# Optimization experiments

Hardware: AMD Instinct MI355X
Metric: run time of the kernel (lower is better)

Reference implementation:

```python
import jax, jax.numpy as jnp
import numpy as np

N = 100000
IN_C = 128
HID = 128
LAT = 64
E = 800000


def gcn_conv(x, src, dst, norm, W, b, num_nodes):
    # x: [N, Cin]; src/dst: [E+N] (self-loops appended); norm: [E+N]
    xw = x @ W                                   # [N, Cout]
    msg = xw[src] * norm[:, None]                # gather + scale, [E+N, Cout]
    out = jax.ops.segment_sum(msg, dst, num_segments=num_nodes)
    return out + b


def setup_inputs() -> dict:
    key = jax.random.key(0)
    ks = jax.random.split(key, 8)
    x = jax.random.normal(ks[0], (N, IN_C), dtype=jnp.float32)
    edge_index = jax.random.randint(ks[1], (2, E), 0, N, dtype=jnp.int64)
    batch = jnp.zeros((N,), dtype=jnp.int64)
    # GCNConv params (Glorot-ish scale)
    W1 = jax.random.normal(ks[2], (IN_C, HID), dtype=jnp.float32) / np.sqrt(IN_C)
    b1 = jnp.zeros((HID,), dtype=jnp.float32)
    Wmu = jax.random.normal(ks[3], (HID, LAT), dtype=jnp.float32) / np.sqrt(HID)
    bmu = jnp.zeros((LAT,), dtype=jnp.float32)
    Wlv = jax.random.normal(ks[4], (HID, LAT), dtype=jnp.float32) / np.sqrt(HID)
    blv = jnp.zeros((LAT,), dtype=jnp.float32)
    return {"x": x, "edge_index": edge_index, "batch": batch,
            "W1": W1, "b1": b1, "Wmu": Wmu, "bmu": bmu, "Wlv": Wlv, "blv": blv}


def reference(x, edge_index, batch, W1, b1, Wmu, bmu, Wlv, blv):
    num_nodes = x.shape[0]
    loop = jnp.arange(num_nodes, dtype=edge_index.dtype)
    src = jnp.concatenate([edge_index[0], loop])   # source nodes (+self loops)
    dst = jnp.concatenate([edge_index[1], loop])   # target nodes (+self loops)
    # symmetric GCN normalization: deg over targets, norm = d[src]^-1/2 * d[dst]^-1/2
    deg = jax.ops.segment_sum(jnp.ones_like(dst, dtype=x.dtype), dst,
                              num_segments=num_nodes)
    dis = jnp.where(deg > 0, jax.lax.rsqrt(deg), 0.0)
    norm = dis[src] * dis[dst]                      # [E+N]

    h = jax.nn.relu(gcn_conv(x, src, dst, norm, W1, b1, num_nodes))
    mu = gcn_conv(h, src, dst, norm, Wmu, bmu, num_nodes)
    logvar = gcn_conv(h, src, dst, norm, Wlv, blv, num_nodes)
    return (mu, logvar)
```

## Files before the change

kernel.cpp:

```cpp
#include <hip/hip_runtime.h>

typedef short bf16x8 __attribute__((ext_vector_type(8)));
typedef float f32x4 __attribute__((ext_vector_type(4)));

#define ELLK 32
#define OCAP 4096
#define CSTRIDE 16

static __device__ __forceinline__ float4 f4zero() { return make_float4(0.f, 0.f, 0.f, 0.f); }

static __device__ __forceinline__ unsigned short f2bf(float f) {
  unsigned u = __float_as_uint(f);
  u += 0x7FFFu + ((u >> 16) & 1u);
  return (unsigned short)(u >> 16);
}
static __device__ __forceinline__ float2 bf2x2(unsigned u) {
  float2 r;
  r.x = __uint_as_float(u << 16);
  r.y = __uint_as_float(u & 0xFFFF0000u);
  return r;
}

__global__ void k_setup(const float* __restrict__ W1, const float* __restrict__ Wmu,
                        const float* __restrict__ Wlv, unsigned short* __restrict__ Wt1,
                        unsigned short* __restrict__ Wt2, uint4* __restrict__ cntz,
                        int* __restrict__ ocount, unsigned* __restrict__ A,
                        unsigned* __restrict__ H, int nz4, int nbz, int n) {
  int b = blockIdx.x;
  if (b < nbz) {
    int i = b * 256 + threadIdx.x;
    if (i < nz4) cntz[i] = make_uint4(0u, 0u, 0u, 0u);
    if (b == 0) {
      int t = threadIdx.x;
      if (t == 0) *ocount = 0;
      if (t < 64) A[(size_t)n * 64 + t] = 0u;
      else if (t < 128) H[(size_t)n * 64 + (t - 64)] = 0u;
    }
  } else {
    int id = (b - nbz) * 256 + threadIdx.x;
    if (id < 16384) {
      int nn = id >> 7, k = id & 127;
      Wt1[id] = f2bf(W1[k * 128 + nn]);
    } else {
      int id2 = id - 16384;
      int nn = id2 >> 7, k = id2 & 127;
      float v = (nn < 64) ? Wmu[k * 64 + nn] : Wlv[k * 64 + (nn - 64)];
      Wt2[id2] = f2bf(v);
    }
  }
}

__global__ void k_fill(const int* __restrict__ ei, int* __restrict__ cnt,
                       int* __restrict__ ell, int2* __restrict__ ovf,
                       int* __restrict__ ocount, int E, int n) {
  int e0 = blockIdx.x * 1024 + threadIdx.x;
  int ss[4], dd[4], pos[4];
  bool ok[4];
#pragma unroll
  for (int k = 0; k < 4; ++k) {
    int e = e0 + k * 256;
    ok[k] = (e < E);
    ss[k] = ok[k] ? ei[e] : 0;
    dd[k] = ok[k] ? ei[E + e] : 0;
  }
#pragma unroll
  for (int k = 0; k < 4; ++k)
    pos[k] = ok[k] ? atomicAdd(&cnt[(size_t)dd[k] * CSTRIDE], 1) : ELLK;
#pragma unroll
  for (int k = 0; k < 4; ++k) {
    if (!ok[k]) continue;
    if (pos[k] < ELLK) {
      __builtin_nontemporal_store(ss[k], &ell[(size_t)pos[k] * n + dd[k]]);
    } else {
      int o = atomicAdd(ocount, 1);
      if (o < OCAP) ovf[o] = make_int2(dd[k], ss[k]);
    }
  }
}

__global__ __launch_bounds__(256) void k_gemm1(
    const float* __restrict__ x, const unsigned short* __restrict__ Wt,
    const int* __restrict__ cnt, unsigned short* __restrict__ A,
    float* __restrict__ dnorm, unsigned* __restrict__ mflag, int n) {
  __shared__ unsigned short Wl[128 * 136];
  __shared__ unsigned short Xl[64 * 136];
  __shared__ float dnl[64];
  const int tid = threadIdx.x;
  const int row0 = blockIdx.x * 64;
  {
    const uint4* Wg = (const uint4*)Wt;
#pragma unroll
    for (int i = 0; i < 8; ++i) {
      int idx = tid + i * 256;
      int r = idx >> 4, c = idx & 15;
      *(uint4*)&Wl[r * 136 + c * 8] = Wg[r * 16 + c];
    }
  }
  {
#pragma unroll
    for (int i = 0; i < 8; ++i) {
      int idx = tid + i * 256;
      int r = idx >> 5, c = idx & 31;
      int gi = row0 + r;
      float4 v = (gi < n) ? ((const float4*)x)[(size_t)gi * 32 + c] : f4zero();
      ushort4 p;
      p.x = f2bf(v.x); p.y = f2bf(v.y); p.z = f2bf(v.z); p.w = f2bf(v.w);
      *(ushort4*)&Xl[r * 136 + c * 4] = p;
    }
  }
  __syncthreads();

  if (tid < 64) {
    int gi = row0 + tid;
    float dn = 0.f;
    if (gi < n) {
      int c = cnt[(size_t)gi * CSTRIDE];
      dn = rsqrtf((float)(c + 1));
      dnorm[gi] = dn;
      int mm = (c < ELLK) ? c : ELLK;
      mflag[gi] = (unsigned)mm | ((c > ELLK) ? 0x80000000u : 0u);
    }
    dnl[tid] = dn;
  }

  const int wave = tid >> 6, lane = tid & 63;
  const int li = lane & 15, quad = lane >> 4;
  const int m0 = wave * 16;
  f32x4 acc[8];
#pragma unroll
  for (int t = 0; t < 8; ++t) acc[t] = (f32x4){0.f, 0.f, 0.f, 0.f};

#pragma unroll
  for (int kk = 0; kk < 4; ++kk) {
    int ko = kk * 32 + quad * 8;
    bf16x8 a = *(const bf16x8*)&Xl[(m0 + li) * 136 + ko];
#pragma unroll
    for (int nt = 0; nt < 8; ++nt) {
      bf16x8 b = *(const bf16x8*)&Wl[(nt * 16 + li) * 136 + ko];
      acc[nt] = __builtin_amdgcn_mfma_f32_16x16x32_bf16(a, b, acc[nt], 0, 0, 0);
    }
  }
  __syncthreads();
  float dn[4];
#pragma unroll
  for (int r = 0; r < 4; ++r) dn[r] = dnl[m0 + quad * 4 + r];
#pragma unroll
  for (int nt = 0; nt < 8; ++nt)
#pragma unroll
    for (int r = 0; r < 4; ++r)
      Xl[(m0 + quad * 4 + r) * 136 + nt * 16 + li] = f2bf(acc[nt][r] * dn[r]);
  __syncthreads();
  {
    uint4* A4 = (uint4*)A;
#pragma unroll
    for (int i = 0; i < 4; ++i) {
      int idx = tid + i * 256;
      int r = idx >> 4, c = idx & 15;
      int gi = row0 + r;
      if (gi < n) A4[(size_t)gi * 16 + c] = *(uint4*)&Xl[r * 136 + c * 8];
    }
  }
}

template <bool EPI_RELU>
__global__ __launch_bounds__(256) void k_spmm(
    const unsigned* __restrict__ mflag, const float* __restrict__ dnorm,
    const int* __restrict__ ell, const int2* __restrict__ ovf,
    const int* __restrict__ ocount, const unsigned* __restrict__ S,
    unsigned* __restrict__ D, const float2* __restrict__ bias, int n) {
  int wid = (blockIdx.x * blockDim.x + threadIdx.x) >> 6;
  if (wid >= n) return;
  int lane = threadIdx.x & 63;

  unsigned mf = mflag[wid];
  int m = (int)(mf & 0xFFFFu);
  float dsd = dnorm[wid];
  float2 acc = bf2x2(S[(size_t)wid * 64 + lane]);

  const int* ep = ell + wid;
  {
    int idx[16];
#pragma unroll
    for (int k = 0; k < 16; ++k) idx[k] = ep[(size_t)k * n];
#pragma unroll
    for (int k = 0; k < 16; ++k) idx[k] = (k < m) ? idx[k] : n;
    unsigned u[16];
#pragma unroll
    for (int k = 0; k < 16; ++k) u[k] = S[(size_t)idx[k] * 64 + lane];
#pragma unroll
    for (int k = 0; k < 16; ++k) {
      float2 f = bf2x2(u[k]);
      acc.x += f.x;
      acc.y += f.y;
    }
  }
  if (m > 16) {
    for (int j0 = 16; j0 < m; j0 += 8) {
      int idx[8];
#pragma unroll
      for (int k = 0; k < 8; ++k) idx[k] = ep[(size_t)(j0 + k) * n];
#pragma unroll
      for (int k = 0; k < 8; ++k) idx[k] = (j0 + k < m) ? idx[k] : n;
      unsigned u[8];
#pragma unroll
      for (int k = 0; k < 8; ++k) u[k] = S[(size_t)idx[k] * 64 + lane];
#pragma unroll
      for (int k = 0; k < 8; ++k) {
        float2 f = bf2x2(u[k]);
        acc.x += f.x;
        acc.y += f.y;
      }
    }
  }
  if (mf & 0x80000000u) {
    int oc = *ocount;
    if (oc > OCAP) oc = OCAP;
    for (int k = 0; k < oc; ++k) {
      int2 e = ovf[k];
      if (e.x == wid) {
        float2 u0 = bf2x2(S[(size_t)e.y * 64 + lane]);
        acc.x += u0.x;
        acc.y += u0.y;
      }
    }
  }
  float2 o;
  if (EPI_RELU) {
    float2 b = bias[lane];
    o.x = dsd * fmaxf(fmaf(dsd, acc.x, b.x), 0.f);
    o.y = dsd * fmaxf(fmaf(dsd, acc.y, b.y), 0.f);
  } else {
    o.x = dsd * acc.x;
    o.y = dsd * acc.y;
  }
  unsigned pk = (unsigned)f2bf(o.x) | ((unsigned)f2bf(o.y) << 16);
  D[(size_t)wid * 64 + lane] = pk;
}

__global__ __launch_bounds__(256) void k_gemm2_mfma(
    const unsigned short* __restrict__ G, const unsigned short* __restrict__ Wt,
    const float* __restrict__ bmu, const float* __restrict__ blv,
    float* __restrict__ out, int n) {
  __shared__ unsigned short Wl[128 * 136];
  __shared__ unsigned short Xl[64 * 136];
  const int tid = threadIdx.x;
  const int row0 = blockIdx.x * 64;
  {
    const uint4* Wg = (const uint4*)Wt;
#pragma unroll
    for (int i = 0; i < 8; ++i) {
      int idx = tid + i * 256;
      int r = idx >> 4, c = idx & 15;
      *(uint4*)&Wl[r * 136 + c * 8] = Wg[r * 16 + c];
    }
  }
  {
    const uint4* Gg = (const uint4*)G;
#pragma unroll
    for (int i = 0; i < 4; ++i) {
      int idx = tid + i * 256;
      int r = idx >> 4, c = idx & 15;
      int gi = row0 + r;
      uint4 v = (gi < n) ? Gg[(size_t)gi * 16 + c] : make_uint4(0, 0, 0, 0);
      *(uint4*)&Xl[r * 136 + c * 8] = v;
    }
  }
  __syncthreads();

  const int wave = tid >> 6, lane = tid & 63;
  const int li = lane & 15, quad = lane >> 4;
  const int m0 = wave * 16;

  float bias[8];
#pragma unroll
  for (int nt = 0; nt < 8; ++nt) {
    int c = nt * 16 + li;
    bias[nt] = (c < 64) ? bmu[c] : blv[c - 64];
  }

  f32x4 acc[8];
#pragma unroll
  for (int t = 0; t < 8; ++t) acc[t] = (f32x4){0.f, 0.f, 0.f, 0.f};

#pragma unroll
  for (int kk = 0; kk < 4; ++kk) {
    int ko = kk * 32 + quad * 8;
    bf16x8 a = *(const bf16x8*)&Xl[(m0 + li) * 136 + ko];
#pragma unroll
    for (int nt = 0; nt < 8; ++nt) {
      bf16x8 b = *(const bf16x8*)&Wl[(nt * 16 + li) * 136 + ko];
      acc[nt] = __builtin_amdgcn_mfma_f32_16x16x32_bf16(a, b, acc[nt], 0, 0, 0);
    }
  }
#pragma unroll
  for (int nt = 0; nt < 8; ++nt) {
    int col = nt * 16 + li;
#pragma unroll
    for (int r = 0; r < 4; ++r) {
      int gi = row0 + m0 + quad * 4 + r;
      if (gi < n) {
        float v = acc[nt][r] + bias[nt];
        if (col < 64) out[(size_t)gi * 64 + col] = v;
        else          out[(size_t)(n + gi) * 64 + (col - 64)] = v;
      }
    }
  }
}

extern "C" void kernel_launch(void* const* d_in, const int* in_sizes, int n_in,
                              void* d_out, int out_size, void* d_ws, size_t ws_size,
                              hipStream_t stream) {
  const float* x   = (const float*)d_in[0];
  const int*   ei  = (const int*)d_in[1];
  const float* W1  = (const float*)d_in[3];
  const float* b1  = (const float*)d_in[4];
  const float* Wmu = (const float*)d_in[5];
  const float* bmu = (const float*)d_in[6];
  const float* Wlv = (const float*)d_in[7];
  const float* blv = (const float*)d_in[8];
  float* out = (float*)d_out;

  const int n = in_sizes[0] / 128;
  const int E = in_sizes[1] / 2;

  float* ws = (float*)d_ws;
  size_t p = 0;
  int* cnt    = (int*)(ws + p); p += (size_t)n * CSTRIDE;
  int* ocount = (int*)(ws + p); p += 1;
  p = (p + 3) & ~(size_t)3;
  int* ell    = (int*)(ws + p); p += (size_t)n * ELLK;
  int2* ovf   = (int2*)(ws + p); p += (size_t)OCAP * 2;
  unsigned* A = (unsigned*)(ws + p); p += (size_t)(n + 1) * 64;
  unsigned* H = (unsigned*)(ws + p); p += (size_t)(n + 1) * 64;
  unsigned* G = (unsigned*)(ws + p); p += (size_t)n * 64;
  unsigned short* Wt1 = (unsigned short*)(ws + p); p += 8192;
  unsigned short* Wt2 = (unsigned short*)(ws + p); p += 8192;
  float* dnorm    = (float*)(ws + p); p += n;
  unsigned* mflag = (unsigned*)(ws + p); p += n;

  int nz4  = (n * CSTRIDE) / 4;
  int nbz  = (nz4 + 255) / 256;
  int eb   = (E + 1023) / 1024;
  int gblk = (n + 63) / 64;
  int sblk = (n + 3) / 4;

  k_setup<<<nbz + 128, 256, 0, stream>>>(W1, Wmu, Wlv, Wt1, Wt2, (uint4*)cnt, ocount,
                                         A, H, nz4, nbz, n);
  k_fill<<<eb, 256, 0, stream>>>(ei, cnt, ell, ovf, ocount, E, n);
  k_gemm1<<<gblk, 256, 0, stream>>>(x, Wt1, cnt, (unsigned short*)A, dnorm, mflag, n);
  k_spmm<true><<<sblk, 256, 0, stream>>>(mflag, dnorm, ell, ovf, ocount, A, H,
                                         (const float2*)b1, n);
  k_spmm<false><<<sblk, 256, 0, stream>>>(mflag, dnorm, ell, ovf, ocount, H, G, nullptr, n);
  k_gemm2_mfma<<<gblk, 256, 0, stream>>>((const unsigned short*)G, Wt2, bmu, blv, out, n);
}
```

Baseline: 294.9 us.

## Fuse edge fill with first GEMM and move source normalization into SpMM

Merges the ELL fill kernel and the first GEMM into one launch, with separate block ranges, so the fill and the dense matmul can run concurrently. Because the GEMM no longer waits for degree counts, the source-side normalization moves into the first SpMM, which gathers dnorm per neighbor, and a small k_dnorm kernel computes norms and flags. Weights are pre-swizzled into MFMA fragment order and read straight from global memory instead of being staged in LDS. The first SpMM loop is simplified to uniform 8-wide batches. The cost is extra dnorm gathers per edge in layer 1 and one added kernel launch.

```diff
diff --git a/kernel.cpp b/kernel.cpp
--- a/kernel.cpp
+++ b/kernel.cpp
@@ -39,63 +39,57 @@
   } else {
     int id = (b - nbz) * 256 + threadIdx.x;
     if (id < 16384) {
-      int nn = id >> 7, k = id & 127;
+      int j = id & 7, lane = (id >> 3) & 63, g = id >> 9;
+      int kk = g >> 3, nt = g & 7, li = lane & 15, quad = lane >> 4;
+      int nn = nt * 16 + li, k = kk * 32 + quad * 8 + j;
       Wt1[id] = f2bf(W1[k * 128 + nn]);
     } else {
       int id2 = id - 16384;
-      int nn = id2 >> 7, k = id2 & 127;
+      int j = id2 & 7, lane = (id2 >> 3) & 63, g = id2 >> 9;
+      int kk = g >> 3, nt = g & 7, li = lane & 15, quad = lane >> 4;
+      int nn = nt * 16 + li, k = kk * 32 + quad * 8 + j;
       float v = (nn < 64) ? Wmu[k * 64 + nn] : Wlv[k * 64 + (nn - 64)];
       Wt2[id2] = f2bf(v);
     }
   }
 }
 
-__global__ void k_fill(const int* __restrict__ ei, int* __restrict__ cnt,
-                       int* __restrict__ ell, int2* __restrict__ ovf,
-                       int* __restrict__ ocount, int E, int n) {
-  int e0 = blockIdx.x * 1024 + threadIdx.x;
-  int ss[4], dd[4], pos[4];
-  bool ok[4];
-#pragma unroll
-  for (int k = 0; k < 4; ++k) {
-    int e = e0 + k * 256;
-    ok[k] = (e < E);
-    ss[k] = ok[k] ? ei[e] : 0;
-    dd[k] = ok[k] ? ei[E + e] : 0;
-  }
-#pragma unroll
-  for (int k = 0; k < 4; ++k)
-    pos[k] = ok[k] ? atomicAdd(&cnt[(size_t)dd[k] * CSTRIDE], 1) : ELLK;
-#pragma unroll
-  for (int k = 0; k < 4; ++k) {
-    if (!ok[k]) continue;
-    if (pos[k] < ELLK) {
-      __builtin_nontemporal_store(ss[k], &ell[(size_t)pos[k] * n + dd[k]]);
-    } else {
-      int o = atomicAdd(ocount, 1);
-      if (o < OCAP) ovf[o] = make_int2(dd[k], ss[k]);
-    }
-  }
-}
-
-__global__ __launch_bounds__(256) void k_gemm1(
+__global__ __launch_bounds__(256, 4) void k_fill_gemm1(
     const float* __restrict__ x, const unsigned short* __restrict__ Wt,
-    const int* __restrict__ cnt, unsigned short* __restrict__ A,
-    float* __restrict__ dnorm, unsigned* __restrict__ mflag, int n) {
-  __shared__ unsigned short Wl[128 * 136];
+    const int* __restrict__ ei, int* __restrict__ cnt, int* __restrict__ ell,
+    int2* __restrict__ ovf, int* __restrict__ ocount,
+    unsigned short* __restrict__ A, int E, int n, int eb) {
   __shared__ unsigned short Xl[64 * 136];
-  __shared__ float dnl[64];
   const int tid = threadIdx.x;
-  const int row0 = blockIdx.x * 64;
-  {
-    const uint4* Wg = (const uint4*)Wt;
-#pragma unroll
-    for (int i = 0; i < 8; ++i) {
-      int idx = tid + i * 256;
-      int r = idx >> 4, c = idx & 15;
-      *(uint4*)&Wl[r * 136 + c * 8] = Wg[r * 16 + c];
-    }
-  }
+
+  if (blockIdx.x < eb) {
+    int e0 = blockIdx.x * 1024 + tid;
+    int ss[4], dd[4], pos[4];
+    bool ok[4];
+#pragma unroll
+    for (int k = 0; k < 4; ++k) {
+      int e = e0 + k * 256;
+      ok[k] = (e < E);
+      ss[k] = ok[k] ? ei[e] : 0;
+      dd[k] = ok[k] ? ei[E + e] : 0;
+    }
+#pragma unroll
+    for (int k = 0; k < 4; ++k)
+      pos[k] = ok[k] ? atomicAdd(&cnt[(size_t)dd[k] * CSTRIDE], 1) : ELLK;
+#pragma unroll
+    for (int k = 0; k < 4; ++k) {
+      if (!ok[k]) continue;
+      if (pos[k] < ELLK) {
+        __builtin_nontemporal_store(ss[k], &ell[(size_t)pos[k] * n + dd[k]]);
+      } else {
+        int o = atomicAdd(ocount, 1);
+        if (o < OCAP) ovf[o] = make_int2(dd[k], ss[k]);
+      }
+    }
+    return;
+  }
+
+  const int row0 = (blockIdx.x - eb) * 64;
   {
 #pragma unroll
     for (int i = 0; i < 8; ++i) {
@@ -110,22 +104,10 @@
   }
   __syncthreads();
 
-  if (tid < 64) {
-    int gi = row0 + tid;
-    float dn = 0.f;
-    if (gi < n) {
-      int c = cnt[(size_t)gi * CSTRIDE];
-      dn = rsqrtf((float)(c + 1));
-      dnorm[gi] = dn;
-      int mm = (c < ELLK) ? c : ELLK;
-      mflag[gi] = (unsigned)mm | ((c > ELLK) ? 0x80000000u : 0u);
-    }
-    dnl[tid] = dn;
-  }
-
   const int wave = tid >> 6, lane = tid & 63;
   const int li = lane & 15, quad = lane >> 4;
   const int m0 = wave * 16;
+  const bf16x8* Wf = (const bf16x8*)Wt;
   f32x4 acc[8];
 #pragma unroll
   for (int t = 0; t < 8; ++t) acc[t] = (f32x4){0.f, 0.f, 0.f, 0.f};
@@ -134,21 +116,19 @@
   for (int kk = 0; kk < 4; ++kk) {
     int ko = kk * 32 + quad * 8;
     bf16x8 a = *(const bf16x8*)&Xl[(m0 + li) * 136 + ko];
-#pragma unroll
-    for (int nt = 0; nt < 8; ++nt) {
-      bf16x8 b = *(const bf16x8*)&Wl[(nt * 16 + li) * 136 + ko];
-      acc[nt] = __builtin_amdgcn_mfma_f32_16x16x32_bf16(a, b, acc[nt], 0, 0, 0);
-    }
+    bf16x8 bf[8];
+#pragma unroll
+    for (int nt = 0; nt < 8; ++nt) bf[nt] = Wf[(kk * 8 + nt) * 64 + lane];
+#pragma unroll
+    for (int nt = 0; nt < 8; ++nt)
+      acc[nt] = __builtin_amdgcn_mfma_f32_16x16x32_bf16(a, bf[nt], acc[nt], 0, 0, 0);
   }
   __syncthreads();
-  float dn[4];
-#pragma unroll
-  for (int r = 0; r < 4; ++r) dn[r] = dnl[m0 + quad * 4 + r];
 #pragma unroll
   for (int nt = 0; nt < 8; ++nt)
 #pragma unroll
     for (int r = 0; r < 4; ++r)
-      Xl[(m0 + quad * 4 + r) * 136 + nt * 16 + li] = f2bf(acc[nt][r] * dn[r]);
+      Xl[(m0 + quad * 4 + r) * 136 + nt * 16 + li] = f2bf(acc[nt][r]);
   __syncthreads();
   {
     uint4* A4 = (uint4*)A;
@@ -162,7 +142,18 @@
   }
 }
 
-template <bool EPI_RELU>
+__global__ void k_dnorm(const int* __restrict__ cnt, float* __restrict__ dnorm,
+                        unsigned* __restrict__ mflag, int n) {
+  int i = blockIdx.x * 256 + threadIdx.x;
+  if (i > n) return;
+  if (i == n) { dnorm[n] = 0.f; mflag[n] = 0u; return; }
+  int c = cnt[(size_t)i * CSTRIDE];
+  dnorm[i] = rsqrtf((float)(c + 1));
+  int m = (c < ELLK) ? c : ELLK;
+  mflag[i] = (unsigned)m | ((c > ELLK) ? 0x80000000u : 0u);
+}
+
+template <bool L1>
 __global__ __launch_bounds__(256) void k_spmm(
     const unsigned* __restrict__ mflag, const float* __restrict__ dnorm,
     const int* __restrict__ ell, const int2* __restrict__ ovf,
@@ -176,40 +167,30 @@
   int m = (int)(mf & 0xFFFFu);
   float dsd = dnorm[wid];
   float2 acc = bf2x2(S[(size_t)wid * 64 + lane]);
+  if (L1) { acc.x *= dsd; acc.y *= dsd; }
 
   const int* ep = ell + wid;
-  {
-    int idx[16];
-#pragma unroll
-    for (int k = 0; k < 16; ++k) idx[k] = ep[(size_t)k * n];
-#pragma unroll
-    for (int k = 0; k < 16; ++k) idx[k] = (k < m) ? idx[k] : n;
-    unsigned u[16];
-#pragma unroll
-    for (int k = 0; k < 16; ++k) u[k] = S[(size_t)idx[k] * 64 + lane];
-#pragma unroll
-    for (int k = 0; k < 16; ++k) {
+  int nbt = (m + 7) >> 3;
+  for (int b = 0; b < nbt; ++b) {
+    int j0 = b * 8;
+    int idx[8];
+#pragma unroll
+    for (int k = 0; k < 8; ++k) idx[k] = ep[(size_t)(j0 + k) * n];
+#pragma unroll
+    for (int k = 0; k < 8; ++k) idx[k] = (j0 + k < m) ? idx[k] : n;
+    unsigned u[8];
+#pragma unroll
+    for (int k = 0; k < 8; ++k) u[k] = S[(size_t)idx[k] * 64 + lane];
+    float w[8];
+    if (L1) {
+#pragma unroll
+      for (int k = 0; k < 8; ++k) w[k] = dnorm[idx[k]];
+    }
+#pragma unroll
+    for (int k = 0; k < 8; ++k) {
       float2 f = bf2x2(u[k]);
-      acc.x += f.x;
-      acc.y += f.y;
-    }
-  }
-  if (m > 16) {
-    for (int j0 = 16; j0 < m; j0 += 8) {
-      int idx[8];
-#pragma unroll
-      for (int k = 0; k < 8; ++k) idx[k] = ep[(size_t)(j0 + k) * n];
-#pragma unroll
-      for (int k = 0; k < 8; ++k) idx[k] = (j0 + k < m) ? idx[k] : n;
-      unsigned u[8];
-#pragma unroll
-      for (int k = 0; k < 8; ++k) u[k] = S[(size_t)idx[k] * 64 + lane];
-#pragma unroll
-      for (int k = 0; k < 8; ++k) {
-        float2 f = bf2x2(u[k]);
-        acc.x += f.x;
-        acc.y += f.y;
-      }
+      if (L1) { acc.x = fmaf(w[k], f.x, acc.x); acc.y = fmaf(w[k], f.y, acc.y); }
+      else    { acc.x += f.x; acc.y += f.y; }
     }
   }
   if (mf & 0x80000000u) {
@@ -219,13 +200,13 @@
       int2 e = ovf[k];
       if (e.x == wid) {
         float2 u0 = bf2x2(S[(size_t)e.y * 64 + lane]);
-        acc.x += u0.x;
-        acc.y += u0.y;
+        float wv = L1 ? dnorm[e.y] : 1.f;
+        acc.x = fmaf(wv, u0.x, acc.x); acc.y = fmaf(wv, u0.y, acc.y);
       }
     }
   }
   float2 o;
-  if (EPI_RELU) {
+  if (L1) {
     float2 b = bias[lane];
     o.x = dsd * fmaxf(fmaf(dsd, acc.x, b.x), 0.f);
     o.y = dsd * fmaxf(fmaf(dsd, acc.y, b.y), 0.f);
@@ -237,23 +218,13 @@
   D[(size_t)wid * 64 + lane] = pk;
 }
 
-__global__ __launch_bounds__(256) void k_gemm2_mfma(
+__global__ __launch_bounds__(256, 4) void k_gemm2_mfma(
     const unsigned short* __restrict__ G, const unsigned short* __restrict__ Wt,
     const float* __restrict__ bmu, const float* __restrict__ blv,
     float* __restrict__ out, int n) {
-  __shared__ unsigned short Wl[128 * 136];
   __shared__ unsigned short Xl[64 * 136];
   const int tid = threadIdx.x;
   const int row0 = blockIdx.x * 64;
-  {
-    const uint4* Wg = (const uint4*)Wt;
-#pragma unroll
-    for (int i = 0; i < 8; ++i) {
-      int idx = tid + i * 256;
-      int r = idx >> 4, c = idx & 15;
-      *(uint4*)&Wl[r * 136 + c * 8] = Wg[r * 16 + c];
-    }
-  }
   {
     const uint4* Gg = (const uint4*)G;
 #pragma unroll
@@ -270,6 +241,7 @@
   const int wave = tid >> 6, lane = tid & 63;
   const int li = lane & 15, quad = lane >> 4;
   const int m0 = wave * 16;
+  const bf16x8* Wf = (const bf16x8*)Wt;
 
   float bias[8];
 #pragma unroll
@@ -286,11 +258,12 @@
   for (int kk = 0; kk < 4; ++kk) {
     int ko = kk * 32 + quad * 8;
     bf16x8 a = *(const bf16x8*)&Xl[(m0 + li) * 136 + ko];
-#pragma unroll
-    for (int nt = 0; nt < 8; ++nt) {
-      bf16x8 b = *(const bf16x8*)&Wl[(nt * 16 + li) * 136 + ko];
-      acc[nt] = __builtin_amdgcn_mfma_f32_16x16x32_bf16(a, b, acc[nt], 0, 0, 0);
-    }
+    bf16x8 bf[8];
+#pragma unroll
+    for (int nt = 0; nt < 8; ++nt) bf[nt] = Wf[(kk * 8 + nt) * 64 + lane];
+#pragma unroll
+    for (int nt = 0; nt < 8; ++nt)
+      acc[nt] = __builtin_amdgcn_mfma_f32_16x16x32_bf16(a, bf[nt], acc[nt], 0, 0, 0);
   }
 #pragma unroll
   for (int nt = 0; nt < 8; ++nt) {
@@ -335,19 +308,21 @@
   unsigned* G = (unsigned*)(ws + p); p += (size_t)n * 64;
   unsigned short* Wt1 = (unsigned short*)(ws + p); p += 8192;
   unsigned short* Wt2 = (unsigned short*)(ws + p); p += 8192;
-  float* dnorm    = (float*)(ws + p); p += n;
-  unsigned* mflag = (unsigned*)(ws + p); p += n;
+  float* dnorm    = (float*)(ws + p); p += n + 1;
+  unsigned* mflag = (unsigned*)(ws + p); p += n + 1;
 
   int nz4  = (n * CSTRIDE) / 4;
   int nbz  = (nz4 + 255) / 256;
   int eb   = (E + 1023) / 1024;
   int gblk = (n + 63) / 64;
+  int nb   = (n + 256) / 256;
   int sblk = (n + 3) / 4;
 
   k_setup<<<nbz + 128, 256, 0, stream>>>(W1, Wmu, Wlv, Wt1, Wt2, (uint4*)cnt, ocount,
                                          A, H, nz4, nbz, n);
-  k_fill<<<eb, 256, 0, stream>>>(ei, cnt, ell, ovf, ocount, E, n);
-  k_gemm1<<<gblk, 256, 0, stream>>>(x, Wt1, cnt, (unsigned short*)A, dnorm, mflag, n);
+  k_fill_gemm1<<<eb + gblk, 256, 0, stream>>>(x, Wt1, ei, cnt, ell, ovf, ocount,
+                                              (unsigned short*)A, E, n, eb);
+  k_dnorm<<<nb, 256, 0, stream>>>(cnt, dnorm, mflag, n);
   k_spmm<true><<<sblk, 256, 0, stream>>>(mflag, dnorm, ell, ovf, ocount, A, H,
                                          (const float2*)b1, n);
   k_spmm<false><<<sblk, 256, 0, stream>>>(mflag, dnorm, ell, ovf, ocount, H, G, nullptr, n);
```

Result: no change. 295.4 us (+0.2%).

## Fuse second SpMM into GEMM2 and pre-swizzle weights into MFMA fragment order

Applied to the files above, without the earlier changes.

The second sparse aggregation is fused into the final GEMM kernel. Each wave aggregates 16 nodes into shared memory and then runs the MFMA projection, which removes the intermediate G buffer write/read and one kernel launch. Weights are pre-permuted in setup into per-lane MFMA fragment order, so both GEMM kernels load B fragments directly from global/L2 instead of staging a 34KB weight tile in LDS. This lowers LDS use to allow more occupancy (launch_bounds 256,4). The cost is that the fused kernel processes nodes serially per wave, giving less memory-level parallelism than one-wave-per-node SpMM. The SpMM loop is also simplified to uniform 8-wide batches.

```diff
diff --git a/kernel.cpp b/kernel.cpp
--- a/kernel.cpp
+++ b/kernel.cpp
@@ -39,11 +39,15 @@
   } else {
     int id = (b - nbz) * 256 + threadIdx.x;
     if (id < 16384) {
-      int nn = id >> 7, k = id & 127;
+      int j = id & 7, lane = (id >> 3) & 63, g = id >> 9;
+      int kk = g >> 3, nt = g & 7, li = lane & 15, quad = lane >> 4;
+      int nn = nt * 16 + li, k = kk * 32 + quad * 8 + j;
       Wt1[id] = f2bf(W1[k * 128 + nn]);
     } else {
       int id2 = id - 16384;
-      int nn = id2 >> 7, k = id2 & 127;
+      int j = id2 & 7, lane = (id2 >> 3) & 63, g = id2 >> 9;
+      int kk = g >> 3, nt = g & 7, li = lane & 15, quad = lane >> 4;
+      int nn = nt * 16 + li, k = kk * 32 + quad * 8 + j;
       float v = (nn < 64) ? Wmu[k * 64 + nn] : Wlv[k * 64 + (nn - 64)];
       Wt2[id2] = f2bf(v);
     }
@@ -78,24 +82,14 @@
   }
 }
 
-__global__ __launch_bounds__(256) void k_gemm1(
+__global__ __launch_bounds__(256, 4) void k_gemm1(
     const float* __restrict__ x, const unsigned short* __restrict__ Wt,
     const int* __restrict__ cnt, unsigned short* __restrict__ A,
     float* __restrict__ dnorm, unsigned* __restrict__ mflag, int n) {
-  __shared__ unsigned short Wl[128 * 136];
   __shared__ unsigned short Xl[64 * 136];
   __shared__ float dnl[64];
   const int tid = threadIdx.x;
   const int row0 = blockIdx.x * 64;
-  {
-    const uint4* Wg = (const uint4*)Wt;
-#pragma unroll
-    for (int i = 0; i < 8; ++i) {
-      int idx = tid + i * 256;
-      int r = idx >> 4, c = idx & 15;
-      *(uint4*)&Wl[r * 136 + c * 8] = Wg[r * 16 + c];
-    }
-  }
   {
 #pragma unroll
     for (int i = 0; i < 8; ++i) {
@@ -108,8 +102,6 @@
       *(ushort4*)&Xl[r * 136 + c * 4] = p;
     }
   }
-  __syncthreads();
-
   if (tid < 64) {
     int gi = row0 + tid;
     float dn = 0.f;
@@ -122,10 +114,12 @@
     }
     dnl[tid] = dn;
   }
+  __syncthreads();
 
   const int wave = tid >> 6, lane = tid & 63;
   const int li = lane & 15, quad = lane >> 4;
   const int m0 = wave * 16;
+  const bf16x8* Wf = (const bf16x8*)Wt;
   f32x4 acc[8];
 #pragma unroll
   for (int t = 0; t < 8; ++t) acc[t] = (f32x4){0.f, 0.f, 0.f, 0.f};
@@ -134,11 +128,12 @@
   for (int kk = 0; kk < 4; ++kk) {
     int ko = kk * 32 + quad * 8;
     bf16x8 a = *(const bf16x8*)&Xl[(m0 + li) * 136 + ko];
-#pragma unroll
-    for (int nt = 0; nt < 8; ++nt) {
-      bf16x8 b = *(const bf16x8*)&Wl[(nt * 16 + li) * 136 + ko];
-      acc[nt] = __builtin_amdgcn_mfma_f32_16x16x32_bf16(a, b, acc[nt], 0, 0, 0);
-    }
+    bf16x8 bf[8];
+#pragma unroll
+    for (int nt = 0; nt < 8; ++nt) bf[nt] = Wf[(kk * 8 + nt) * 64 + lane];
+#pragma unroll
+    for (int nt = 0; nt < 8; ++nt)
+      acc[nt] = __builtin_amdgcn_mfma_f32_16x16x32_bf16(a, bf[nt], acc[nt], 0, 0, 0);
   }
   __syncthreads();
   float dn[4];
@@ -162,8 +157,7 @@
   }
 }
 
-template <bool EPI_RELU>
-__global__ __launch_bounds__(256) void k_spmm(
+__global__ __launch_bounds__(256) void k_spmm1(
     const unsigned* __restrict__ mflag, const float* __restrict__ dnorm,
     const int* __restrict__ ell, const int2* __restrict__ ovf,
     const int* __restrict__ ocount, const unsigned* __restrict__ S,
@@ -178,38 +172,22 @@
   float2 acc = bf2x2(S[(size_t)wid * 64 + lane]);
 
   const int* ep = ell + wid;
-  {
-    int idx[16];
-#pragma unroll
-    for (int k = 0; k < 16; ++k) idx[k] = ep[(size_t)k * n];
-#pragma unroll
-    for (int k = 0; k < 16; ++k) idx[k] = (k < m) ? idx[k] : n;
-    unsigned u[16];
-#pragma unroll
-    for (int k = 0; k < 16; ++k) u[k] = S[(size_t)idx[k] * 64 + lane];
-#pragma unroll
-    for (int k = 0; k < 16; ++k) {
+  int nbt = (m + 7) >> 3;
+  for (int b = 0; b < nbt; ++b) {
+    int j0 = b * 8;
+    int idx[8];
+#pragma unroll
+    for (int k = 0; k < 8; ++k) idx[k] = ep[(size_t)(j0 + k) * n];
+#pragma unroll
+    for (int k = 0; k < 8; ++k) idx[k] = (j0 + k < m) ? idx[k] : n;
+    unsigned u[8];
+#pragma unroll
+    for (int k = 0; k < 8; ++k) u[k] = S[(size_t)idx[k] * 64 + lane];
+#pragma unroll
+    for (int k = 0; k < 8; ++k) {
       float2 f = bf2x2(u[k]);
       acc.x += f.x;
       acc.y += f.y;
-    }
-  }
-  if (m > 16) {
-    for (int j0 = 16; j0 < m; j0 += 8) {
-      int idx[8];
-#pragma unroll
-      for (int k = 0; k < 8; ++k) idx[k] = ep[(size_t)(j0 + k) * n];
-#pragma unroll
-      for (int k = 0; k < 8; ++k) idx[k] = (j0 + k < m) ? idx[k] : n;
-      unsigned u[8];
-#pragma unroll
-      for (int k = 0; k < 8; ++k) u[k] = S[(size_t)idx[k] * 64 + lane];
-#pragma unroll
-      for (int k = 0; k < 8; ++k) {
-        float2 f = bf2x2(u[k]);
-        acc.x += f.x;
-        acc.y += f.y;
-      }
     }
   }
   if (mf & 0x80000000u) {
@@ -224,52 +202,77 @@
       }
     }
   }
+  float2 b = bias[lane];
   float2 o;
-  if (EPI_RELU) {
-    float2 b = bias[lane];
-    o.x = dsd * fmaxf(fmaf(dsd, acc.x, b.x), 0.f);
-    o.y = dsd * fmaxf(fmaf(dsd, acc.y, b.y), 0.f);
-  } else {
-    o.x = dsd * acc.x;
-    o.y = dsd * acc.y;
-  }
+  o.x = dsd * fmaxf(fmaf(dsd, acc.x, b.x), 0.f);
+  o.y = dsd * fmaxf(fmaf(dsd, acc.y, b.y), 0.f);
   unsigned pk = (unsigned)f2bf(o.x) | ((unsigned)f2bf(o.y) << 16);
   D[(size_t)wid * 64 + lane] = pk;
 }
 
-__global__ __launch_bounds__(256) void k_gemm2_mfma(
-    const unsigned short* __restrict__ G, const unsigned short* __restrict__ Wt,
-    const float* __restrict__ bmu, const float* __restrict__ blv,
-    float* __restrict__ out, int n) {
-  __shared__ unsigned short Wl[128 * 136];
+__global__ __launch_bounds__(256, 4) void k_spmm2_gemm2(
+    const unsigned* __restrict__ mflag, const float* __restrict__ dnorm,
+    const int* __restrict__ ell, const int2* __restrict__ ovf,
+    const int* __restrict__ ocount, const unsigned* __restrict__ H,
+    const unsigned short* __restrict__ Wt, const float* __restrict__ bmu,
+    const float* __restrict__ blv, float* __restrict__ out, int n) {
   __shared__ unsigned short Xl[64 * 136];
   const int tid = threadIdx.x;
+  const int wave = tid >> 6, lane = tid & 63;
   const int row0 = blockIdx.x * 64;
-  {
-    const uint4* Wg = (const uint4*)Wt;
-#pragma unroll
-    for (int i = 0; i < 8; ++i) {
-      int idx = tid + i * 256;
-      int r = idx >> 4, c = idx & 15;
-      *(uint4*)&Wl[r * 136 + c * 8] = Wg[r * 16 + c];
-    }
-  }
-  {
-    const uint4* Gg = (const uint4*)G;
-#pragma unroll
-    for (int i = 0; i < 4; ++i) {
-      int idx = tid + i * 256;
-      int r = idx >> 4, c = idx & 15;
-      int gi = row0 + r;
-      uint4 v = (gi < n) ? Gg[(size_t)gi * 16 + c] : make_uint4(0, 0, 0, 0);
-      *(uint4*)&Xl[r * 136 + c * 8] = v;
-    }
+
+#pragma unroll 1
+  for (int i = 0; i < 16; ++i) {
+    int nd = row0 + wave * 16 + i;
+    unsigned pk = 0u;
+    if (nd < n) {
+      unsigned mf = mflag[nd];
+      int m = (int)(mf & 0xFFFFu);
+      float dsd = dnorm[nd];
+      float2 acc = bf2x2(H[(size_t)nd * 64 + lane]);
+      const int* ep = ell + nd;
+      int nbt = (m + 7) >> 3;
+      for (int b = 0; b < nbt; ++b) {
+        int j0 = b * 8;
+        int idx[8];
+#pragma unroll
+        for (int k = 0; k < 8; ++k) idx[k] = ep[(size_t)(j0 + k) * n];
+#pragma unroll
+        for (int k = 0; k < 8; ++k) idx[k] = (j0 + k < m) ? idx[k] : n;
+        unsigned u[8];
+#pragma unroll
+        for (int k = 0; k < 8; ++k) u[k] = H[(size_t)idx[k] * 64 + lane];
+#pragma unroll
+        for (int k = 0; k < 8; ++k) {
+          float2 f = bf2x2(u[k]);
+          acc.x += f.x;
+          acc.y += f.y;
+        }
+      }
+      if (mf & 0x80000000u) {
+        int oc = *ocount;
+        if (oc > OCAP) oc = OCAP;
+        for (int k = 0; k < oc; ++k) {
+          int2 e = ovf[k];
+          if (e.x == nd) {
+            float2 u0 = bf2x2(H[(size_t)e.y * 64 + lane]);
+            acc.x += u0.x;
+            acc.y += u0.y;
+          }
+        }
+      }
+      float2 o;
+      o.x = dsd * acc.x;
+      o.y = dsd * acc.y;
+      pk = (unsigned)f2bf(o.x) | ((unsigned)f2bf(o.y) << 16);
+    }
+    *(unsigned*)&Xl[(wave * 16 + i) * 136 + 2 * lane] = pk;
   }
   __syncthreads();
 
-  const int wave = tid >> 6, lane = tid & 63;
   const int li = lane & 15, quad = lane >> 4;
   const int m0 = wave * 16;
+  const bf16x8* Wf = (const bf16x8*)Wt;
 
   float bias[8];
 #pragma unroll
@@ -286,11 +289,12 @@
   for (int kk = 0; kk < 4; ++kk) {
     int ko = kk * 32 + quad * 8;
     bf16x8 a = *(const bf16x8*)&Xl[(m0 + li) * 136 + ko];
-#pragma unroll
-    for (int nt = 0; nt < 8; ++nt) {
-      bf16x8 b = *(const bf16x8*)&Wl[(nt * 16 + li) * 136 + ko];
-      acc[nt] = __builtin_amdgcn_mfma_f32_16x16x32_bf16(a, b, acc[nt], 0, 0, 0);
-    }
+    bf16x8 bf[8];
+#pragma unroll
+    for (int nt = 0; nt < 8; ++nt) bf[nt] = Wf[(kk * 8 + nt) * 64 + lane];
+#pragma unroll
+    for (int nt = 0; nt < 8; ++nt)
+      acc[nt] = __builtin_amdgcn_mfma_f32_16x16x32_bf16(a, bf[nt], acc[nt], 0, 0, 0);
   }
 #pragma unroll
   for (int nt = 0; nt < 8; ++nt) {
@@ -332,7 +336,6 @@
   int2* ovf   = (int2*)(ws + p); p += (size_t)OCAP * 2;
   unsigned* A = (unsigned*)(ws + p); p += (size_t)(n + 1) * 64;
   unsigned* H = (unsigned*)(ws + p); p += (size_t)(n + 1) * 64;
-  unsigned* G = (unsigned*)(ws + p); p += (size_t)n * 64;
   unsigned short* Wt1 = (unsigned short*)(ws + p); p += 8192;
   unsigned short* Wt2 = (unsigned short*)(ws + p); p += 8192;
   float* dnorm    = (float*)(ws + p); p += n;
@@ -348,8 +351,8 @@
                                          A, H, nz4, nbz, n);
   k_fill<<<eb, 256, 0, stream>>>(ei, cnt, ell, ovf, ocount, E, n);
   k_gemm1<<<gblk, 256, 0, stream>>>(x, Wt1, cnt, (unsigned short*)A, dnorm, mflag, n);
-  k_spmm<true><<<sblk, 256, 0, stream>>>(mflag, dnorm, ell, ovf, ocount, A, H,
-                                         (const float2*)b1, n);
-  k_spmm<false><<<sblk, 256, 0, stream>>>(mflag, dnorm, ell, ovf, ocount, H, G, nullptr, n);
-  k_gemm2_mfma<<<gblk, 256, 0, stream>>>((const unsigned short*)G, Wt2, bmu, blv, out, n);
-}
+  k_spmm1<<<sblk, 256, 0, stream>>>(mflag, dnorm, ell, ovf, ocount, A, H,
+                                    (const float2*)b1, n);
+  k_spmm2_gemm2<<<gblk, 256, 0, stream>>>(mflag, dnorm, ell, ovf, ocount, H, Wt2,
+                                          bmu, blv, out, n);
+}
```

New measurement: 282.6 us. 4.2% less time.
